# Performance work log

Measured on AMD Instinct MI355X. Metric: run time of the kernel, lower is better.

## Reference

```python
import jax, jax.numpy as jnp
import numpy as np

B, S, N1, N2, NS = 2048, 1024, 8192, 16384, 256
EPS = 1e-10

def setup_inputs() -> dict:
    key = jax.random.key(0)
    ks = jax.random.split(key, 12)
    t_in = jax.random.uniform(ks[0], (B,), jnp.float32)
    y_in = jax.random.uniform(ks[1], (B, S), jnp.float32)
    den_gas = jax.random.uniform(ks[2], (B, 1), jnp.float32) * 1e4
    alpha_1st = jax.random.uniform(ks[3], (N1,), jnp.float32)
    gamma_1st = jax.random.uniform(ks[4], (N1,), jnp.float32) * 50.0
    alpha_2nd = jax.random.uniform(ks[5], (N2,), jnp.float32)
    gamma_2nd = jax.random.uniform(ks[6], (N2,), jnp.float32) * 50.0
    r1_1st = jax.random.randint(ks[7], (N1,), 0, S, jnp.int32)
    p_1st = jax.random.randint(ks[8], (N1,), 0, S, jnp.int32)
    r1_2nd = jax.random.randint(ks[9], (N2,), 0, S, jnp.int32)
    r2_2nd = jax.random.randint(ks[10], (N2,), 0, S, jnp.int32)
    p_2nd = jax.random.randint(ks[11], (N2,), 0, S, jnp.int32)
    inds_surf = 512 + jnp.arange(NS, dtype=jnp.int32)  # surface species slots
    inds_mant = 768 + jnp.arange(NS, dtype=jnp.int32)  # mantle species slots
    return dict(t_in=t_in, y_in=y_in, den_gas=den_gas,
                alpha_1st=alpha_1st, gamma_1st=gamma_1st,
                alpha_2nd=alpha_2nd, gamma_2nd=gamma_2nd,
                r1_1st=r1_1st, p_1st=p_1st,
                r1_2nd=r1_2nd, r2_2nd=r2_2nd, p_2nd=p_2nd,
                inds_surf=inds_surf, inds_mant=inds_mant)

def reference(t_in, y_in, den_gas, alpha_1st, gamma_1st, alpha_2nd, gamma_2nd,
              r1_1st, p_1st, r1_2nd, r2_2nd, p_2nd, inds_surf, inds_mant):
    zeros = jnp.zeros_like(y_in)
    # medium parameters (module_med): temperature from t, den_norm from den_gas
    T = 10.0 + 5.0 * jax.nn.sigmoid(t_in)[:, None]            # [B,1]
    # rmod_1st / rmod_2nd: modified-Arrhenius rate coefficients
    rates_1st = alpha_1st[None, :] * jnp.exp(-gamma_1st[None, :] / T)      # [B,N1]
    rates_2nd = (alpha_2nd[None, :] * jnp.sqrt(T / 300.0)
                 * jnp.exp(-gamma_2nd[None, :] / T))                       # [B,N2]
    # reaction fluxes (gather)
    terms_1st = rates_1st * y_in[:, r1_1st]                                 # [B,N1]
    terms_2nd = rates_2nd * y_in[:, r1_2nd] * y_in[:, r2_2nd] * den_gas     # [B,N2]
    # surface gain / loss assemblers (gain-only and loss-only scatters)
    gain = (zeros.at[:, p_1st].add(terms_1st)
                 .at[:, p_2nd].add(terms_2nd))[:, inds_surf]
    loss = (zeros.at[:, r1_1st].add(-terms_1st)
                 .at[:, r1_2nd].add(-terms_2nd)
                 .at[:, r2_2nd].add(-terms_2nd))[:, inds_surf]
    dy_surf_gain = jnp.sum(gain, axis=-1, keepdims=True)    # [B,1] >= 0
    dy_surf_loss = -jnp.sum(loss, axis=-1, keepdims=True)   # [B,1] >= 0
    # rmod_smt: surface<->mantle transfer coefficients (three-phase)
    y_surf_tot = jnp.sum(y_in[:, inds_surf], axis=-1, keepdims=True)
    y_mant_tot = jnp.sum(y_in[:, inds_mant], axis=-1, keepdims=True)
    k_s2m = dy_surf_gain / (y_surf_tot + EPS)  # burial rate per surface species
    k_m2s = dy_surf_loss / (y_mant_tot + EPS)  # excavation rate per mantle species
    terms_s2m = k_s2m * y_in[:, inds_surf]     # [B,NS]
    terms_m2s = k_m2s * y_in[:, inds_mant]     # [B,NS]
    # full RHS: asm_smt + asm_1st + asm_2nd
    dy = (zeros
          .at[:, p_1st].add(terms_1st).at[:, r1_1st].add(-terms_1st)
          .at[:, p_2nd].add(terms_2nd)
          .at[:, r1_2nd].add(-terms_2nd).at[:, r2_2nd].add(-terms_2nd)
          .at[:, inds_surf].add(terms_m2s - terms_s2m)
          .at[:, inds_mant].add(terms_s2m - terms_m2s))
    return dy
```

## Files before the change

kernel.cpp:

```cpp
#include <hip/hip_runtime.h>
#include <hip/hip_fp16.h>

constexpr int kB  = 2048;
constexpr int kS  = 1024;
constexpr int kN1 = 8192;
constexpr int kN2 = 16384;
constexpr int kNTERM = kN1 + kN2;
constexpr int kQT    = kNTERM / 4;
constexpr int kRoles = 2*kN1 + 3*kN2;
constexpr float kEPS = 1e-10f;
constexpr int NT = 256;

constexpr int kPitchE   = 48;
constexpr int kChunks   = kPitchE / 8;
constexpr int kGrpWords = kChunks * kS * 4;
constexpr int kEllWords = 4 * kGrpWords;

constexpr size_t kOffCnt  = 0;
constexpr size_t kOffCur  = 16384;
constexpr size_t kOffEll  = 32768;
constexpr size_t kOffSpOf = kOffEll + (size_t)kEllWords * 4;
constexpr size_t kOffPsOf = kOffSpOf + 4096;
constexpr size_t kOffRec  = kOffPsOf + 4096;
constexpr size_t kMemset  = kOffSpOf;
constexpr size_t kWsNeed  = kOffRec + (size_t)kNTERM * 16;

__device__ __forceinline__ void role_decode(
    int i, const int* r1_1, const int* p_1, const int* r1_2,
    const int* r2_2, const int* p_2, int& s, int& j, bool& neg)
{
    if (i < kN1)                { j = i;       s = p_1[j];  neg = false; }
    else if (i < 2*kN1)         { j = i - kN1; s = r1_1[j]; neg = true;  }
    else if (i < 2*kN1 + kN2)   { int q = i - 2*kN1;         j = kN1 + q; s = p_2[q];  neg = false; }
    else if (i < 2*kN1 + 2*kN2) { int q = i - 2*kN1 - kN2;   j = kN1 + q; s = r1_2[q]; neg = true; }
    else                        { int q = i - 2*kN1 - 2*kN2; j = kN1 + q; s = r2_2[q]; neg = true; }
}

__global__ __launch_bounds__(NT) void count_fill(
    const float* __restrict__ a1, const float* __restrict__ g1,
    const float* __restrict__ a2, const float* __restrict__ g2,
    const int* __restrict__ r1_1, const int* __restrict__ p_1,
    const int* __restrict__ r1_2, const int* __restrict__ r2_2,
    const int* __restrict__ p_2,
    unsigned* __restrict__ cntQ, float4* __restrict__ rec)
{
    int i = blockIdx.x * NT + threadIdx.x;
    if (i >= kRoles) return;
    int s, j; bool neg;
    role_decode(i, r1_1, p_1, r1_2, r2_2, p_2, s, j, neg);
    atomicAdd(&cntQ[(j / kQT) * kS + s], 1u);
    if (i < kNTERM) {
        float4 r;
        if (i < kN1) { r.x = a1[i]; r.y = -g1[i]; r.z = __int_as_float(r1_1[i]); r.w = 0.f; }
        else { int q = i - kN1; r.x = a2[q]; r.y = -g2[q];
               r.z = __int_as_float(r1_2[q]); r.w = __int_as_float(r2_2[q]); }
        rec[i] = r;
    }
}

__global__ __launch_bounds__(1024) void balance_sort(
    const unsigned* __restrict__ cntQ,
    unsigned* __restrict__ sp_of_pos, unsigned* __restrict__ pos_of_sp)
{
    __shared__ unsigned keys[kS];
    int tid = threadIdx.x;
    unsigned tot = cntQ[tid] + cntQ[kS + tid] + cntQ[2*kS + tid] + cntQ[3*kS + tid];
    unsigned cat = (tid < 512) ? 0u : (tid < 768 ? 1u : 2u);
    keys[tid] = (cat << 20) | (tot << 10) | (unsigned)tid;
    __syncthreads();
    for (int k = 2; k <= kS; k <<= 1) {
        for (int jj = k >> 1; jj > 0; jj >>= 1) {
            int ixj = tid ^ jj;
            if (ixj > tid) {
                unsigned a = keys[tid], b = keys[ixj];
                bool up = ((tid & k) == 0);
                if ((a > b) == up) { keys[tid] = b; keys[ixj] = a; }
            }
            __syncthreads();
        }
    }
    unsigned sp = keys[tid] & 1023u;
    sp_of_pos[tid] = sp;
    pos_of_sp[sp] = (unsigned)tid;
}

__global__ __launch_bounds__(NT) void ell_fill(
    const int* __restrict__ r1_1, const int* __restrict__ p_1,
    const int* __restrict__ r1_2, const int* __restrict__ r2_2,
    const int* __restrict__ p_2,
    const unsigned* __restrict__ pos_of_sp,
    unsigned* __restrict__ curC, unsigned* __restrict__ ell)
{
    int i = blockIdx.x * NT + threadIdx.x;
    if (i >= kRoles) return;
    int s, j; bool neg;
    role_decode(i, r1_1, p_1, r1_2, r2_2, p_2, s, j, neg);
    int q = j / kQT;
    unsigned p = pos_of_sp[s];
    unsigned e = ((unsigned)(j - q * kQT + 1) << 2) | (neg ? 0x8000u : 0u);
    unsigned k = atomicAdd(&curC[q * kS + p], 1u);
    if (k < (unsigned)kPitchE) {
        unsigned w = (unsigned)(q * kGrpWords)
                   + ((k >> 3) * (unsigned)kS + p) * 4u + ((k >> 1) & 3u);
        atomicOr(&ell[w], e << ((k & 1u) * 16u));
    }
}

template<bool TRACK>
__device__ __forceinline__ void accum8s(
    uint4 e, const __half2* __restrict__ t2,
    float& r0, float& r1, float& a0, float& a1)
{
    const char* tb = (const char*)t2;
    #pragma unroll
    for (int w = 0; w < 4; ++w) {
        unsigned u = (&e.x)[w];
        #pragma unroll
        for (int hh = 0; hh < 2; ++hh) {
            unsigned h = (hh == 0) ? (u & 0xffffu) : (u >> 16);
            unsigned t = *(const unsigned*)(tb + (h & 0x7fffu));
            unsigned m = (h & 0x8000u) * 0x10001u;
            unsigned ts = t ^ m;
            float2 f = __half22float2(*(const __half2*)&ts);
            r0 += f.x; r1 += f.y;
            if (TRACK) {
                float2 g = __half22float2(*(const __half2*)&t);
                a0 += g.x; a1 += g.y;
            }
        }
    }
}

__global__ __launch_bounds__(NT, 4) void three_phase_gather6(
    const float* __restrict__ t_in, const float* __restrict__ y_in,
    const float* __restrict__ den_gas,
    const unsigned* __restrict__ curC, const unsigned* __restrict__ ell,
    const unsigned* __restrict__ sp_of_pos,
    const float4* __restrict__ rec, float* __restrict__ dy)
{
    __shared__ float2  y2[kS];
    __shared__ __half2 terms2[kQT + 1];
    __shared__ float   red[4][8];

    const int tid = threadIdx.x;
    const int b0  = blockIdx.x * 2;

    {
        const float4* s0 = (const float4*)(y_in + (size_t)b0 * kS);
        const float4* s1 = (const float4*)(y_in + (size_t)(b0 + 1) * kS);
        float4 va = s0[tid], vb = s1[tid];
        y2[4*tid+0] = make_float2(va.x, vb.x);
        y2[4*tid+1] = make_float2(va.y, vb.y);
        y2[4*tid+2] = make_float2(va.z, vb.z);
        y2[4*tid+3] = make_float2(va.w, vb.w);
    }
    if (tid == 0) terms2[0] = __halves2half2(__float2half(0.f), __float2half(0.f));

    unsigned sp[4];
    #pragma unroll
    for (int slot = 0; slot < 4; ++slot) sp[slot] = sp_of_pos[tid + slot * NT];

    float T0 = 10.f + 5.f / (1.f + __expf(-t_in[b0]));
    float T1 = 10.f + 5.f / (1.f + __expf(-t_in[b0 + 1]));
    float i0 = 1.f / T0, i1 = 1.f / T1;
    float c20 = __fsqrt_rn(T0 * (1.f / 300.f)) * den_gas[b0];
    float c21 = __fsqrt_rn(T1 * (1.f / 300.f)) * den_gas[b0 + 1];

    float acc[4][2] = {};
    float ab2[2] = {};

    #pragma unroll
    for (int q = 0; q < 4; ++q) {
        __syncthreads();
        const int base = q * kQT;
        #pragma unroll 2
        for (int it = 0; it < kQT / NT; ++it) {
            int j = base + it * NT + tid;
            float4 r = rec[j];
            float al = r.x, ng = r.y;
            int ra = __float_as_int(r.z), rb = __float_as_int(r.w);
            float t0, t1;
            if (j < kN1) {
                float2 ya = y2[ra];
                t0 = al * __expf(ng * i0) * ya.x;
                t1 = al * __expf(ng * i1) * ya.y;
            } else {
                float2 ya = y2[ra], yb = y2[rb];
                t0 = c20 * al * __expf(ng * i0) * ya.x * yb.x;
                t1 = c21 * al * __expf(ng * i1) * ya.y * yb.y;
            }
            terms2[j - base + 1] = __halves2half2(__float2half(t0), __float2half(t1));
        }
        const unsigned* cq = curC + q * kS;
        const uint4* bq = (const uint4*)(ell + q * kGrpWords);
        uint4 pf[4]; int cc[4];
        #pragma unroll
        for (int slot = 0; slot < 4; ++slot) {
            int p = tid + slot * NT;
            int c = (int)cq[p]; cc[slot] = c < kPitchE ? c : kPitchE;
            pf[slot] = bq[p];
        }
        __syncthreads();
        #pragma unroll
        for (int slot = 0; slot < 4; ++slot) {
            int p = tid + slot * NT;
            float s0 = 0.f, s1 = 0.f, r0 = 0.f, r1 = 0.f;
            if (slot == 2) accum8s<true >(pf[slot], terms2, s0, s1, r0, r1);
            else           accum8s<false>(pf[slot], terms2, s0, s1, r0, r1);
            int trips = (cc[slot] + 7) >> 3;
            const uint4* ap = bq + p + kS;
            for (int t = 1; t < trips; ++t) {
                uint4 e = *ap; ap += kS;
                if (slot == 2) accum8s<true >(e, terms2, s0, s1, r0, r1);
                else           accum8s<false>(e, terms2, s0, s1, r0, r1);
            }
            acc[slot][0] += s0; acc[slot][1] += s1;
            if (slot == 2) { ab2[0] += r0; ab2[1] += r1; }
        }
    }

    float gn0 = 0.5f * (ab2[0] + acc[2][0]), ls0 = 0.5f * (ab2[0] - acc[2][0]);
    float gn1 = 0.5f * (ab2[1] + acc[2][1]), ls1 = 0.5f * (ab2[1] - acc[2][1]);

    float ys0 = y2[512 + tid].x, ys1 = y2[512 + tid].y;
    float ym0 = y2[768 + tid].x, ym1 = y2[768 + tid].y;
    float v[8] = {gn0, ls0, ys0, ym0, gn1, ls1, ys1, ym1};
    #pragma unroll
    for (int off = 32; off > 0; off >>= 1) {
        #pragma unroll
        for (int w = 0; w < 8; ++w) v[w] += __shfl_down(v[w], off, 64);
    }
    int wave = tid >> 6;
    if ((tid & 63) == 0) {
        #pragma unroll
        for (int w = 0; w < 8; ++w) red[wave][w] = v[w];
    }
    __syncthreads();
    float tv[8];
    #pragma unroll
    for (int w = 0; w < 8; ++w) tv[w] = red[0][w] + red[1][w] + red[2][w] + red[3][w];

    float ks2m0 = tv[0] / (tv[2] + kEPS), km2s0 = tv[1] / (tv[3] + kEPS);
    float ks2m1 = tv[4] / (tv[6] + kEPS), km2s1 = tv[5] / (tv[7] + kEPS);

    float* o0 = dy + (size_t)b0 * kS;
    float* o1 = o0 + kS;
    o0[sp[0]] = acc[0][0];  o1[sp[0]] = acc[0][1];
    o0[sp[1]] = acc[1][0];  o1[sp[1]] = acc[1][1];
    {
        unsigned s2 = sp[2];
        float2 yss = y2[s2], ymm = y2[s2 + 256];
        o0[s2] = acc[2][0] + km2s0 * ymm.x - ks2m0 * yss.x;
        o1[s2] = acc[2][1] + km2s1 * ymm.y - ks2m1 * yss.y;
    }
    {
        unsigned s3 = sp[3];
        float2 yss = y2[s3 - 256], ymm = y2[s3];
        o0[s3] = acc[3][0] + ks2m0 * yss.x - km2s0 * ymm.x;
        o1[s3] = acc[3][1] + ks2m1 * yss.y - km2s1 * ymm.y;
    }
}

__global__ __launch_bounds__(NT) void three_phase_scatter(
    const float* __restrict__ t_in, const float* __restrict__ y_in,
    const float* __restrict__ den_gas,
    const float* __restrict__ alpha_1st, const float* __restrict__ gamma_1st,
    const float* __restrict__ alpha_2nd, const float* __restrict__ gamma_2nd,
    const int* __restrict__ r1_1st, const int* __restrict__ p_1st,
    const int* __restrict__ r1_2nd, const int* __restrict__ r2_2nd,
    const int* __restrict__ p_2nd, float* __restrict__ dy)
{
    __shared__ float y_row[kS];
    __shared__ float accs[kS];
    __shared__ float tot[4];
    const int tid = threadIdx.x;
    const int b   = blockIdx.x;
    ((float4*)y_row)[tid] = ((const float4*)(y_in + (size_t)b * kS))[tid];
    ((float4*)accs)[tid] = make_float4(0.f, 0.f, 0.f, 0.f);
    if (tid < 4) tot[tid] = 0.f;
    float t = t_in[b];
    float T = 10.f + 5.f / (1.f + __expf(-t));
    float invT = 1.f / T, sqT = __fsqrt_rn(T * (1.f / 300.f)), dg = den_gas[b];
    __syncthreads();
    float gain = 0.f, loss = 0.f;
    for (int j = tid; j < kN1; j += NT) {
        int r1 = r1_1st[j], p = p_1st[j];
        float term = alpha_1st[j] * __expf(-gamma_1st[j] * invT) * y_row[r1];
        atomicAdd(&accs[p], term); atomicAdd(&accs[r1], -term);
        if ((unsigned)(p - 512) < 256u) gain += term;
        if ((unsigned)(r1 - 512) < 256u) loss += term;
    }
    for (int j = tid; j < kN2; j += NT) {
        int r1 = r1_2nd[j], r2 = r2_2nd[j], p = p_2nd[j];
        float term = sqT * dg * alpha_2nd[j] * __expf(-gamma_2nd[j] * invT) * y_row[r1] * y_row[r2];
        atomicAdd(&accs[p], term); atomicAdd(&accs[r1], -term); atomicAdd(&accs[r2], -term);
        if ((unsigned)(p - 512) < 256u) gain += term;
        if ((unsigned)(r1 - 512) < 256u) loss += term;
        if ((unsigned)(r2 - 512) < 256u) loss += term;
    }
    float g = gain, l = loss;
    #pragma unroll
    for (int off = 32; off > 0; off >>= 1) { g += __shfl_down(g, off, 64); l += __shfl_down(l, off, 64); }
    if ((tid & 63) == 0) { atomicAdd(&tot[0], g); atomicAdd(&tot[1], l); }
    __syncthreads();
    if (tid < 64) {
        float a2v = 0.f;
        for (int u = tid; u < 256; u += 64) a2v += y_row[512 + u];
        #pragma unroll
        for (int off = 32; off > 0; off >>= 1) a2v += __shfl_down(a2v, off, 64);
        if (tid == 0) tot[2] = a2v;
    } else if (tid < 128) {
        float m2 = 0.f;
        for (int u = tid - 64; u < 256; u += 64) m2 += y_row[768 + u];
        #pragma unroll
        for (int off = 32; off > 0; off >>= 1) m2 += __shfl_down(m2, off, 64);
        if (tid == 64) tot[3] = m2;
    }
    __syncthreads();
    float k_s2m = tot[0] / (tot[2] + kEPS);
    float k_m2s = tot[1] / (tot[3] + kEPS);
    float* out = dy + (size_t)b * kS;
    for (int s = tid; s < kS; s += NT) {
        float v = accs[s];
        if ((unsigned)(s - 512) < 256u) v += k_m2s * y_row[s + 256] - k_s2m * y_row[s];
        else if (s >= 768)              v += k_s2m * y_row[s - 256] - k_m2s * y_row[s];
        out[s] = v;
    }
}

extern "C" void kernel_launch(void* const* d_in, const int* in_sizes, int n_in,
                              void* d_out, int out_size, void* d_ws, size_t ws_size,
                              hipStream_t stream) {
    const float* t_in      = (const float*)d_in[0];
    const float* y_in      = (const float*)d_in[1];
    const float* den_gas   = (const float*)d_in[2];
    const float* alpha_1st = (const float*)d_in[3];
    const float* gamma_1st = (const float*)d_in[4];
    const float* alpha_2nd = (const float*)d_in[5];
    const float* gamma_2nd = (const float*)d_in[6];
    const int*   r1_1st    = (const int*)d_in[7];
    const int*   p_1st     = (const int*)d_in[8];
    const int*   r1_2nd    = (const int*)d_in[9];
    const int*   r2_2nd    = (const int*)d_in[10];
    const int*   p_2nd     = (const int*)d_in[11];
    float* dy = (float*)d_out;

    if (ws_size >= kWsNeed) {
        char* ws = (char*)d_ws;
        unsigned* cntQ      = (unsigned*)(ws + kOffCnt);
        unsigned* curC      = (unsigned*)(ws + kOffCur);
        unsigned* ell       = (unsigned*)(ws + kOffEll);
        unsigned* sp_of_pos = (unsigned*)(ws + kOffSpOf);
        unsigned* pos_of_sp = (unsigned*)(ws + kOffPsOf);
        float4*   rec       = (float4*)  (ws + kOffRec);
        hipMemsetAsync(ws, 0, kMemset, stream);
        count_fill<<<kRoles / NT, NT, 0, stream>>>(
            alpha_1st, gamma_1st, alpha_2nd, gamma_2nd,
            r1_1st, p_1st, r1_2nd, r2_2nd, p_2nd, cntQ, rec);
        balance_sort<<<1, 1024, 0, stream>>>(cntQ, sp_of_pos, pos_of_sp);
        ell_fill<<<kRoles / NT, NT, 0, stream>>>(
            r1_1st, p_1st, r1_2nd, r2_2nd, p_2nd, pos_of_sp, curC, ell);
        three_phase_gather6<<<kB / 2, NT, 0, stream>>>(
            t_in, y_in, den_gas, curC, ell, sp_of_pos, rec, dy);
    } else {
        three_phase_scatter<<<kB, NT, 0, stream>>>(
            t_in, y_in, den_gas, alpha_1st, gamma_1st, alpha_2nd, gamma_2nd,
            r1_1st, p_1st, r1_2nd, r2_2nd, p_2nd, dy);
    }
}
```

Measured before the change: 166.8 us.

## Replace memset and bitonic sort with single-block counting-sort rank kernel

```diff
diff --git a/kernel.cpp b/kernel.cpp
--- a/kernel.cpp
+++ b/kernel.cpp
@@ -12,17 +12,15 @@
 constexpr int NT = 256;
 
 constexpr int kPitchE   = 48;
-constexpr int kChunks   = kPitchE / 8;
-constexpr int kGrpWords = kChunks * kS * 4;
-constexpr int kEllWords = 4 * kGrpWords;
-
-constexpr size_t kOffCnt  = 0;
-constexpr size_t kOffCur  = 16384;
-constexpr size_t kOffEll  = 32768;
-constexpr size_t kOffSpOf = kOffEll + (size_t)kEllWords * 4;
-constexpr size_t kOffPsOf = kOffSpOf + 4096;
-constexpr size_t kOffRec  = kOffPsOf + 4096;
-constexpr size_t kMemset  = kOffSpOf;
+constexpr int kGrpU16   = kPitchE * kS;
+constexpr int kEllU16   = 4 * kGrpU16;
+
+constexpr size_t kOffSpOf = 0;
+constexpr size_t kOffPsOf = 4096;
+constexpr size_t kOffCQP  = 8192;
+constexpr size_t kOffCur  = 24576;
+constexpr size_t kOffEll  = 40960;
+constexpr size_t kOffRec  = kOffEll + (size_t)kEllU16 * 2;
 constexpr size_t kWsNeed  = kOffRec + (size_t)kNTERM * 16;
 
 __device__ __forceinline__ void role_decode(
@@ -36,60 +34,63 @@
     else                        { int q = i - 2*kN1 - 2*kN2; j = kN1 + q; s = r2_2[q]; neg = true; }
 }
 
-__global__ __launch_bounds__(NT) void count_fill(
+__global__ __launch_bounds__(1024) void build_rank(
+    const int* __restrict__ r1_1, const int* __restrict__ p_1,
+    const int* __restrict__ r1_2, const int* __restrict__ r2_2,
+    const int* __restrict__ p_2,
+    unsigned* __restrict__ sp_of_pos, unsigned* __restrict__ pos_of_sp,
+    unsigned* __restrict__ cntQP, unsigned* __restrict__ curC)
+{
+    __shared__ unsigned cnt[4 * kS];
+    __shared__ unsigned hist[768];
+    __shared__ unsigned pref[768];
+    __shared__ unsigned cur[768];
+    const int tid = threadIdx.x;
+
+    for (int i = tid; i < 4 * kS; i += 1024) cnt[i] = 0;
+    if (tid < 768) { hist[tid] = 0; cur[tid] = 0; }
+    __syncthreads();
+
+    for (int i = tid; i < kRoles; i += 1024) {
+        int s, j; bool neg;
+        role_decode(i, r1_1, p_1, r1_2, r2_2, p_2, s, j, neg);
+        atomicAdd(&cnt[(j / kQT) * kS + s], 1u);
+    }
+    __syncthreads();
+
+    unsigned tot = cnt[tid] + cnt[kS + tid] + cnt[2*kS + tid] + cnt[3*kS + tid];
+    unsigned cat = (tid < 512) ? 0u : (tid < 768 ? 1u : 2u);
+    unsigned bin = cat * 256 + (tot > 255u ? 255u : tot);
+    atomicAdd(&hist[bin], 1u);
+    __syncthreads();
+
+    if (tid < 768) pref[tid] = hist[tid];
+    __syncthreads();
+    for (int off = 1; off < 768; off <<= 1) {
+        unsigned t = 0;
+        if (tid < 768 && tid >= off) t = pref[tid - off];
+        __syncthreads();
+        if (tid < 768) pref[tid] += t;
+        __syncthreads();
+    }
+    unsigned off_in = atomicAdd(&cur[bin], 1u);
+    unsigned pos = pref[bin] - hist[bin] + off_in;
+    pos_of_sp[tid] = pos;
+    sp_of_pos[pos] = (unsigned)tid;
+    #pragma unroll
+    for (int q = 0; q < 4; ++q) cntQP[q * kS + pos] = cnt[q * kS + tid];
+    for (int i = tid; i < 4 * kS; i += 1024) curC[i] = 0;
+}
+
+__global__ __launch_bounds__(NT) void ell_fill(
     const float* __restrict__ a1, const float* __restrict__ g1,
     const float* __restrict__ a2, const float* __restrict__ g2,
     const int* __restrict__ r1_1, const int* __restrict__ p_1,
     const int* __restrict__ r1_2, const int* __restrict__ r2_2,
     const int* __restrict__ p_2,
-    unsigned* __restrict__ cntQ, float4* __restrict__ rec)
-{
-    int i = blockIdx.x * NT + threadIdx.x;
-    if (i >= kRoles) return;
-    int s, j; bool neg;
-    role_decode(i, r1_1, p_1, r1_2, r2_2, p_2, s, j, neg);
-    atomicAdd(&cntQ[(j / kQT) * kS + s], 1u);
-    if (i < kNTERM) {
-        float4 r;
-        if (i < kN1) { r.x = a1[i]; r.y = -g1[i]; r.z = __int_as_float(r1_1[i]); r.w = 0.f; }
-        else { int q = i - kN1; r.x = a2[q]; r.y = -g2[q];
-               r.z = __int_as_float(r1_2[q]); r.w = __int_as_float(r2_2[q]); }
-        rec[i] = r;
-    }
-}
-
-__global__ __launch_bounds__(1024) void balance_sort(
-    const unsigned* __restrict__ cntQ,
-    unsigned* __restrict__ sp_of_pos, unsigned* __restrict__ pos_of_sp)
-{
-    __shared__ unsigned keys[kS];
-    int tid = threadIdx.x;
-    unsigned tot = cntQ[tid] + cntQ[kS + tid] + cntQ[2*kS + tid] + cntQ[3*kS + tid];
-    unsigned cat = (tid < 512) ? 0u : (tid < 768 ? 1u : 2u);
-    keys[tid] = (cat << 20) | (tot << 10) | (unsigned)tid;
-    __syncthreads();
-    for (int k = 2; k <= kS; k <<= 1) {
-        for (int jj = k >> 1; jj > 0; jj >>= 1) {
-            int ixj = tid ^ jj;
-            if (ixj > tid) {
-                unsigned a = keys[tid], b = keys[ixj];
-                bool up = ((tid & k) == 0);
-                if ((a > b) == up) { keys[tid] = b; keys[ixj] = a; }
-            }
-            __syncthreads();
-        }
-    }
-    unsigned sp = keys[tid] & 1023u;
-    sp_of_pos[tid] = sp;
-    pos_of_sp[sp] = (unsigned)tid;
-}
-
-__global__ __launch_bounds__(NT) void ell_fill(
-    const int* __restrict__ r1_1, const int* __restrict__ p_1,
-    const int* __restrict__ r1_2, const int* __restrict__ r2_2,
-    const int* __restrict__ p_2,
     const unsigned* __restrict__ pos_of_sp,
-    unsigned* __restrict__ curC, unsigned* __restrict__ ell)
+    unsigned* __restrict__ curC, unsigned short* __restrict__ ell,
+    float4* __restrict__ rec)
 {
     int i = blockIdx.x * NT + threadIdx.x;
     if (i >= kRoles) return;
@@ -97,44 +98,52 @@
     role_decode(i, r1_1, p_1, r1_2, r2_2, p_2, s, j, neg);
     int q = j / kQT;
     unsigned p = pos_of_sp[s];
-    unsigned e = ((unsigned)(j - q * kQT + 1) << 2) | (neg ? 0x8000u : 0u);
+    unsigned short e = (unsigned short)(((j - q * kQT + 1) << 2) | (neg ? 0x8000u : 0u));
     unsigned k = atomicAdd(&curC[q * kS + p], 1u);
-    if (k < (unsigned)kPitchE) {
-        unsigned w = (unsigned)(q * kGrpWords)
-                   + ((k >> 3) * (unsigned)kS + p) * 4u + ((k >> 1) & 3u);
-        atomicOr(&ell[w], e << ((k & 1u) * 16u));
+    if (k < (unsigned)kPitchE)
+        ell[(unsigned)(q * kGrpU16) + (k >> 3) * (unsigned)(kS * 8) + p * 8u + (k & 7u)] = e;
+
+    if (i < kNTERM) {
+        float4 r;
+        if (i < kN1) { r.x = a1[i]; r.y = -g1[i]; r.z = __int_as_float(r1_1[i]); r.w = 0.f; }
+        else { int u = i - kN1; r.x = a2[u]; r.y = -g2[u];
+               r.z = __int_as_float(r1_2[u]); r.w = __int_as_float(r2_2[u]); }
+        rec[i] = r;
     }
 }
 
 template<bool TRACK>
-__device__ __forceinline__ void accum8s(
-    uint4 e, const __half2* __restrict__ t2,
+__device__ __forceinline__ void accum8m(
+    uint4 e, int valid, const __half2* __restrict__ t2,
     float& r0, float& r1, float& a0, float& a1)
 {
     const char* tb = (const char*)t2;
     #pragma unroll
     for (int w = 0; w < 4; ++w) {
         unsigned u = (&e.x)[w];
-        #pragma unroll
-        for (int hh = 0; hh < 2; ++hh) {
-            unsigned h = (hh == 0) ? (u & 0xffffu) : (u >> 16);
-            unsigned t = *(const unsigned*)(tb + (h & 0x7fffu));
-            unsigned m = (h & 0x8000u) * 0x10001u;
-            unsigned ts = t ^ m;
-            float2 f = __half22float2(*(const __half2*)&ts);
-            r0 += f.x; r1 += f.y;
-            if (TRACK) {
-                float2 g = __half22float2(*(const __half2*)&t);
-                a0 += g.x; a1 += g.y;
-            }
+        unsigned h0 = u & 0xffffu;
+        unsigned h1 = u >> 16;
+        h0 = (2*w     < valid) ? h0 : 0u;
+        h1 = (2*w + 1 < valid) ? h1 : 0u;
+        unsigned t0 = *(const unsigned*)(tb + (h0 & 0x7fffu));
+        unsigned t1 = *(const unsigned*)(tb + (h1 & 0x7fffu));
+        unsigned ts0 = t0 ^ ((h0 & 0x8000u) * 0x10001u);
+        unsigned ts1 = t1 ^ ((h1 & 0x8000u) * 0x10001u);
+        float2 f0 = __half22float2(*(const __half2*)&ts0);
+        float2 f1 = __half22float2(*(const __half2*)&ts1);
+        r0 += f0.x + f1.x; r1 += f0.y + f1.y;
+        if (TRACK) {
+            float2 g0 = __half22float2(*(const __half2*)&t0);
+            float2 g1v = __half22float2(*(const __half2*)&t1);
+            a0 += g0.x + g1v.x; a1 += g0.y + g1v.y;
         }
     }
 }
 
-__global__ __launch_bounds__(NT, 4) void three_phase_gather6(
+__global__ __launch_bounds__(NT, 4) void three_phase_gather7(
     const float* __restrict__ t_in, const float* __restrict__ y_in,
     const float* __restrict__ den_gas,
-    const unsigned* __restrict__ curC, const unsigned* __restrict__ ell,
+    const unsigned* __restrict__ cntQP, const unsigned short* __restrict__ ell,
     const unsigned* __restrict__ sp_of_pos,
     const float4* __restrict__ rec, float* __restrict__ dy)
 {
@@ -191,8 +200,8 @@
             }
             terms2[j - base + 1] = __halves2half2(__float2half(t0), __float2half(t1));
         }
-        const unsigned* cq = curC + q * kS;
-        const uint4* bq = (const uint4*)(ell + q * kGrpWords);
+        const unsigned* cq = cntQP + q * kS;
+        const uint4* bq = (const uint4*)(ell + q * kGrpU16);
         uint4 pf[4]; int cc[4];
         #pragma unroll
         for (int slot = 0; slot < 4; ++slot) {
@@ -204,15 +213,18 @@
         #pragma unroll
         for (int slot = 0; slot < 4; ++slot) {
             int p = tid + slot * NT;
+            int c = cc[slot];
             float s0 = 0.f, s1 = 0.f, r0 = 0.f, r1 = 0.f;
-            if (slot == 2) accum8s<true >(pf[slot], terms2, s0, s1, r0, r1);
-            else           accum8s<false>(pf[slot], terms2, s0, s1, r0, r1);
-            int trips = (cc[slot] + 7) >> 3;
+            int v0 = c > 8 ? 8 : c;
+            if (slot == 2) accum8m<true >(pf[slot], v0, terms2, s0, s1, r0, r1);
+            else           accum8m<false>(pf[slot], v0, terms2, s0, s1, r0, r1);
+            int trips = (c + 7) >> 3;
             const uint4* ap = bq + p + kS;
             for (int t = 1; t < trips; ++t) {
                 uint4 e = *ap; ap += kS;
-                if (slot == 2) accum8s<true >(e, terms2, s0, s1, r0, r1);
-                else           accum8s<false>(e, terms2, s0, s1, r0, r1);
+                int vt = c - 8 * t; vt = vt > 8 ? 8 : vt;
+                if (slot == 2) accum8m<true >(e, vt, terms2, s0, s1, r0, r1);
+                else           accum8m<false>(e, vt, terms2, s0, s1, r0, r1);
             }
             acc[slot][0] += s0; acc[slot][1] += s1;
             if (slot == 2) { ab2[0] += r0; ab2[1] += r1; }
@@ -347,21 +359,21 @@
 
     if (ws_size >= kWsNeed) {
         char* ws = (char*)d_ws;
-        unsigned* cntQ      = (unsigned*)(ws + kOffCnt);
-        unsigned* curC      = (unsigned*)(ws + kOffCur);
-        unsigned* ell       = (unsigned*)(ws + kOffEll);
-        unsigned* sp_of_pos = (unsigned*)(ws + kOffSpOf);
-        unsigned* pos_of_sp = (unsigned*)(ws + kOffPsOf);
-        float4*   rec       = (float4*)  (ws + kOffRec);
-        hipMemsetAsync(ws, 0, kMemset, stream);
-        count_fill<<<kRoles / NT, NT, 0, stream>>>(
+        unsigned*       sp_of_pos = (unsigned*)(ws + kOffSpOf);
+        unsigned*       pos_of_sp = (unsigned*)(ws + kOffPsOf);
+        unsigned*       cntQP     = (unsigned*)(ws + kOffCQP);
+        unsigned*       curC      = (unsigned*)(ws + kOffCur);
+        unsigned short* ell       = (unsigned short*)(ws + kOffEll);
+        float4*         rec       = (float4*)(ws + kOffRec);
+        build_rank<<<1, 1024, 0, stream>>>(
+            r1_1st, p_1st, r1_2nd, r2_2nd, p_2nd,
+            sp_of_pos, pos_of_sp, cntQP, curC);
+        ell_fill<<<kRoles / NT, NT, 0, stream>>>(
             alpha_1st, gamma_1st, alpha_2nd, gamma_2nd,
-            r1_1st, p_1st, r1_2nd, r2_2nd, p_2nd, cntQ, rec);
-        balance_sort<<<1, 1024, 0, stream>>>(cntQ, sp_of_pos, pos_of_sp);
-        ell_fill<<<kRoles / NT, NT, 0, stream>>>(
-            r1_1st, p_1st, r1_2nd, r2_2nd, p_2nd, pos_of_sp, curC, ell);
-        three_phase_gather6<<<kB / 2, NT, 0, stream>>>(
-            t_in, y_in, den_gas, curC, ell, sp_of_pos, rec, dy);
+            r1_1st, p_1st, r1_2nd, r2_2nd, p_2nd,
+            pos_of_sp, curC, ell, rec);
+        three_phase_gather7<<<kB / 2, NT, 0, stream>>>(
+            t_in, y_in, den_gas, cntQP, ell, sp_of_pos, rec, dy);
     } else {
         three_phase_scatter<<<kB, NT, 0, stream>>>(
             t_in, y_in, den_gas, alpha_1st, gamma_1st, alpha_2nd, gamma_2nd,
```

Result: slower. 186.3 us (+11.7%).

## Drop species balance sort and fuse record build into ELL fill

Applied to the files above, without the earlier changes.

```diff
diff --git a/kernel.cpp b/kernel.cpp
--- a/kernel.cpp
+++ b/kernel.cpp
@@ -12,17 +12,13 @@
 constexpr int NT = 256;
 
 constexpr int kPitchE   = 48;
-constexpr int kChunks   = kPitchE / 8;
-constexpr int kGrpWords = kChunks * kS * 4;
-constexpr int kEllWords = 4 * kGrpWords;
-
-constexpr size_t kOffCnt  = 0;
-constexpr size_t kOffCur  = 16384;
-constexpr size_t kOffEll  = 32768;
-constexpr size_t kOffSpOf = kOffEll + (size_t)kEllWords * 4;
-constexpr size_t kOffPsOf = kOffSpOf + 4096;
-constexpr size_t kOffRec  = kOffPsOf + 4096;
-constexpr size_t kMemset  = kOffSpOf;
+constexpr int kGrpU16   = kPitchE * kS;
+constexpr int kEllU16   = 4 * kGrpU16;
+
+constexpr size_t kOffCur  = 0;
+constexpr size_t kOffEll  = 16384;
+constexpr size_t kOffRec  = kOffEll + (size_t)kEllU16 * 2;
+constexpr size_t kMemset  = kOffRec;
 constexpr size_t kWsNeed  = kOffRec + (size_t)kNTERM * 16;
 
 __device__ __forceinline__ void role_decode(
@@ -36,73 +32,32 @@
     else                        { int q = i - 2*kN1 - 2*kN2; j = kN1 + q; s = r2_2[q]; neg = true; }
 }
 
-__global__ __launch_bounds__(NT) void count_fill(
+__global__ __launch_bounds__(NT) void ell_fill(
     const float* __restrict__ a1, const float* __restrict__ g1,
     const float* __restrict__ a2, const float* __restrict__ g2,
     const int* __restrict__ r1_1, const int* __restrict__ p_1,
     const int* __restrict__ r1_2, const int* __restrict__ r2_2,
     const int* __restrict__ p_2,
-    unsigned* __restrict__ cntQ, float4* __restrict__ rec)
-{
-    int i = blockIdx.x * NT + threadIdx.x;
-    if (i >= kRoles) return;
-    int s, j; bool neg;
-    role_decode(i, r1_1, p_1, r1_2, r2_2, p_2, s, j, neg);
-    atomicAdd(&cntQ[(j / kQT) * kS + s], 1u);
-    if (i < kNTERM) {
-        float4 r;
-        if (i < kN1) { r.x = a1[i]; r.y = -g1[i]; r.z = __int_as_float(r1_1[i]); r.w = 0.f; }
-        else { int q = i - kN1; r.x = a2[q]; r.y = -g2[q];
-               r.z = __int_as_float(r1_2[q]); r.w = __int_as_float(r2_2[q]); }
-        rec[i] = r;
-    }
-}
-
-__global__ __launch_bounds__(1024) void balance_sort(
-    const unsigned* __restrict__ cntQ,
-    unsigned* __restrict__ sp_of_pos, unsigned* __restrict__ pos_of_sp)
-{
-    __shared__ unsigned keys[kS];
-    int tid = threadIdx.x;
-    unsigned tot = cntQ[tid] + cntQ[kS + tid] + cntQ[2*kS + tid] + cntQ[3*kS + tid];
-    unsigned cat = (tid < 512) ? 0u : (tid < 768 ? 1u : 2u);
-    keys[tid] = (cat << 20) | (tot << 10) | (unsigned)tid;
-    __syncthreads();
-    for (int k = 2; k <= kS; k <<= 1) {
-        for (int jj = k >> 1; jj > 0; jj >>= 1) {
-            int ixj = tid ^ jj;
-            if (ixj > tid) {
-                unsigned a = keys[tid], b = keys[ixj];
-                bool up = ((tid & k) == 0);
-                if ((a > b) == up) { keys[tid] = b; keys[ixj] = a; }
-            }
-            __syncthreads();
-        }
-    }
-    unsigned sp = keys[tid] & 1023u;
-    sp_of_pos[tid] = sp;
-    pos_of_sp[sp] = (unsigned)tid;
-}
-
-__global__ __launch_bounds__(NT) void ell_fill(
-    const int* __restrict__ r1_1, const int* __restrict__ p_1,
-    const int* __restrict__ r1_2, const int* __restrict__ r2_2,
-    const int* __restrict__ p_2,
-    const unsigned* __restrict__ pos_of_sp,
-    unsigned* __restrict__ curC, unsigned* __restrict__ ell)
+    unsigned* __restrict__ curC, unsigned short* __restrict__ ell,
+    float4* __restrict__ rec)
 {
     int i = blockIdx.x * NT + threadIdx.x;
     if (i >= kRoles) return;
     int s, j; bool neg;
     role_decode(i, r1_1, p_1, r1_2, r2_2, p_2, s, j, neg);
     int q = j / kQT;
-    unsigned p = pos_of_sp[s];
-    unsigned e = ((unsigned)(j - q * kQT + 1) << 2) | (neg ? 0x8000u : 0u);
-    unsigned k = atomicAdd(&curC[q * kS + p], 1u);
-    if (k < (unsigned)kPitchE) {
-        unsigned w = (unsigned)(q * kGrpWords)
-                   + ((k >> 3) * (unsigned)kS + p) * 4u + ((k >> 1) & 3u);
-        atomicOr(&ell[w], e << ((k & 1u) * 16u));
+    unsigned short e = (unsigned short)(((j - q * kQT + 1) << 2) | (neg ? 0x8000u : 0u));
+    unsigned k = atomicAdd(&curC[q * kS + s], 1u);
+    if (k < (unsigned)kPitchE)
+        ell[(unsigned)(q * kGrpU16) + (k >> 3) * (unsigned)(kS * 8)
+            + (unsigned)s * 8u + (k & 7u)] = e;
+
+    if (i < kNTERM) {
+        float4 r;
+        if (i < kN1) { r.x = a1[i]; r.y = -g1[i]; r.z = __int_as_float(r1_1[i]); r.w = 0.f; }
+        else { int u = i - kN1; r.x = a2[u]; r.y = -g2[u];
+               r.z = __int_as_float(r1_2[u]); r.w = __int_as_float(r2_2[u]); }
+        rec[i] = r;
     }
 }
 
@@ -119,8 +74,7 @@
         for (int hh = 0; hh < 2; ++hh) {
             unsigned h = (hh == 0) ? (u & 0xffffu) : (u >> 16);
             unsigned t = *(const unsigned*)(tb + (h & 0x7fffu));
-            unsigned m = (h & 0x8000u) * 0x10001u;
-            unsigned ts = t ^ m;
+            unsigned ts = t ^ ((h & 0x8000u) * 0x10001u);
             float2 f = __half22float2(*(const __half2*)&ts);
             r0 += f.x; r1 += f.y;
             if (TRACK) {
@@ -131,11 +85,10 @@
     }
 }
 
-__global__ __launch_bounds__(NT, 4) void three_phase_gather6(
+__global__ __launch_bounds__(NT, 4) void three_phase_gather10(
     const float* __restrict__ t_in, const float* __restrict__ y_in,
     const float* __restrict__ den_gas,
-    const unsigned* __restrict__ curC, const unsigned* __restrict__ ell,
-    const unsigned* __restrict__ sp_of_pos,
+    const unsigned* __restrict__ curC, const unsigned short* __restrict__ ell,
     const float4* __restrict__ rec, float* __restrict__ dy)
 {
     __shared__ float2  y2[kS];
@@ -155,10 +108,6 @@
         y2[4*tid+3] = make_float2(va.w, vb.w);
     }
     if (tid == 0) terms2[0] = __halves2half2(__float2half(0.f), __float2half(0.f));
-
-    unsigned sp[4];
-    #pragma unroll
-    for (int slot = 0; slot < 4; ++slot) sp[slot] = sp_of_pos[tid + slot * NT];
 
     float T0 = 10.f + 5.f / (1.f + __expf(-t_in[b0]));
     float T1 = 10.f + 5.f / (1.f + __expf(-t_in[b0 + 1]));
@@ -192,23 +141,23 @@
             terms2[j - base + 1] = __halves2half2(__float2half(t0), __float2half(t1));
         }
         const unsigned* cq = curC + q * kS;
-        const uint4* bq = (const uint4*)(ell + q * kGrpWords);
+        const uint4* bq = (const uint4*)(ell + q * kGrpU16);
         uint4 pf[4]; int cc[4];
         #pragma unroll
         for (int slot = 0; slot < 4; ++slot) {
-            int p = tid + slot * NT;
-            int c = (int)cq[p]; cc[slot] = c < kPitchE ? c : kPitchE;
-            pf[slot] = bq[p];
+            int s = tid + slot * NT;
+            int c = (int)cq[s]; cc[slot] = c < kPitchE ? c : kPitchE;
+            pf[slot] = bq[s];
         }
         __syncthreads();
         #pragma unroll
         for (int slot = 0; slot < 4; ++slot) {
-            int p = tid + slot * NT;
+            int s = tid + slot * NT;
             float s0 = 0.f, s1 = 0.f, r0 = 0.f, r1 = 0.f;
             if (slot == 2) accum8s<true >(pf[slot], terms2, s0, s1, r0, r1);
             else           accum8s<false>(pf[slot], terms2, s0, s1, r0, r1);
             int trips = (cc[slot] + 7) >> 3;
-            const uint4* ap = bq + p + kS;
+            const uint4* ap = bq + s + kS;
             for (int t = 1; t < trips; ++t) {
                 uint4 e = *ap; ap += kS;
                 if (slot == 2) accum8s<true >(e, terms2, s0, s1, r0, r1);
@@ -245,20 +194,14 @@
 
     float* o0 = dy + (size_t)b0 * kS;
     float* o1 = o0 + kS;
-    o0[sp[0]] = acc[0][0];  o1[sp[0]] = acc[0][1];
-    o0[sp[1]] = acc[1][0];  o1[sp[1]] = acc[1][1];
-    {
-        unsigned s2 = sp[2];
-        float2 yss = y2[s2], ymm = y2[s2 + 256];
-        o0[s2] = acc[2][0] + km2s0 * ymm.x - ks2m0 * yss.x;
-        o1[s2] = acc[2][1] + km2s1 * ymm.y - ks2m1 * yss.y;
-    }
-    {
-        unsigned s3 = sp[3];
-        float2 yss = y2[s3 - 256], ymm = y2[s3];
-        o0[s3] = acc[3][0] + ks2m0 * yss.x - km2s0 * ymm.x;
-        o1[s3] = acc[3][1] + ks2m1 * yss.y - km2s1 * ymm.y;
-    }
+    o0[tid]       = acc[0][0];
+    o0[tid + 256] = acc[1][0];
+    o0[tid + 512] = acc[2][0] + km2s0 * ym0 - ks2m0 * ys0;
+    o0[tid + 768] = acc[3][0] + ks2m0 * ys0 - km2s0 * ym0;
+    o1[tid]       = acc[0][1];
+    o1[tid + 256] = acc[1][1];
+    o1[tid + 512] = acc[2][1] + km2s1 * ym1 - ks2m1 * ys1;
+    o1[tid + 768] = acc[3][1] + ks2m1 * ys1 - km2s1 * ym1;
 }
 
 __global__ __launch_bounds__(NT) void three_phase_scatter(
@@ -347,21 +290,15 @@
 
     if (ws_size >= kWsNeed) {
         char* ws = (char*)d_ws;
-        unsigned* cntQ      = (unsigned*)(ws + kOffCnt);
-        unsigned* curC      = (unsigned*)(ws + kOffCur);
-        unsigned* ell       = (unsigned*)(ws + kOffEll);
-        unsigned* sp_of_pos = (unsigned*)(ws + kOffSpOf);
-        unsigned* pos_of_sp = (unsigned*)(ws + kOffPsOf);
-        float4*   rec       = (float4*)  (ws + kOffRec);
+        unsigned*       curC = (unsigned*)(ws + kOffCur);
+        unsigned short* ell  = (unsigned short*)(ws + kOffEll);
+        float4*         rec  = (float4*)(ws + kOffRec);
         hipMemsetAsync(ws, 0, kMemset, stream);
-        count_fill<<<kRoles / NT, NT, 0, stream>>>(
+        ell_fill<<<kRoles / NT, NT, 0, stream>>>(
             alpha_1st, gamma_1st, alpha_2nd, gamma_2nd,
-            r1_1st, p_1st, r1_2nd, r2_2nd, p_2nd, cntQ, rec);
-        balance_sort<<<1, 1024, 0, stream>>>(cntQ, sp_of_pos, pos_of_sp);
-        ell_fill<<<kRoles / NT, NT, 0, stream>>>(
-            r1_1st, p_1st, r1_2nd, r2_2nd, p_2nd, pos_of_sp, curC, ell);
-        three_phase_gather6<<<kB / 2, NT, 0, stream>>>(
-            t_in, y_in, den_gas, curC, ell, sp_of_pos, rec, dy);
+            r1_1st, p_1st, r1_2nd, r2_2nd, p_2nd, curC, ell, rec);
+        three_phase_gather10<<<kB / 2, NT, 0, stream>>>(
+            t_in, y_in, den_gas, curC, ell, rec, dy);
     } else {
         three_phase_scatter<<<kB, NT, 0, stream>>>(
             t_in, y_in, den_gas, alpha_1st, gamma_1st, alpha_2nd, gamma_2nd,
```

Measured after the change: 152.3 us. 8.7% less time.
